# Kernel optimization log

Measured on AMD Instinct MI355X. Metric: run time of the kernel, lower is better.

The kernel has to match this reference:

```python
import jax, jax.numpy as jnp
import numpy as np

N, C, HW, HEADS = 2048, 16, 8, 4
F = C * HW * HW  # 1024
E = 16384
EPS = 1e-5
NEG_SLOPE = 0.2


def _bn(x, g, b):
    # training-mode BatchNorm2d over (N, H, W)
    m = x.mean(axis=(0, 2, 3), keepdims=True)
    v = x.var(axis=(0, 2, 3), keepdims=True)
    return (x - m) * jax.lax.rsqrt(v + EPS) * g[None, :, None, None] + b[None, :, None, None]


def _conv1x1(x, w, b):
    # 1x1 conv == per-pixel linear: w is [out_c, in_c]
    return jnp.einsum('nchw,oc->nohw', x, w) + b[None, :, None, None]


def _gatv2(xf, edge_index, wl, bl, wr, br, att, bias_gat):
    # xf: [N, F] node features
    xl = (xf @ wl + bl).reshape(N, HEADS, F)  # source-side transform (lin_l)
    xr = (xf @ wr + br).reshape(N, HEADS, F)  # target-side transform (lin_r)
    src, dst = edge_index[0], edge_index[1]
    loops = jnp.arange(N)
    # PyG default: remove existing self loops (mask them) then add self loops
    src_f = jnp.concatenate([src, loops])
    dst_f = jnp.concatenate([dst, loops])
    valid = jnp.concatenate([src != dst, jnp.ones((N,), bool)])
    xj = xl[src_f]                                   # [E+N, HEADS, F] gather
    e = jax.nn.leaky_relu(xj + xr[dst_f], negative_slope=NEG_SLOPE)
    logits = jnp.einsum('ehf,hf->eh', e, att)        # [E+N, HEADS]
    logits = jnp.where(valid[:, None], logits, -jnp.inf)
    mx = jax.lax.stop_gradient(jax.ops.segment_max(logits, dst_f, num_segments=N))
    expv = jnp.where(valid[:, None], jnp.exp(logits - mx[dst_f]), 0.0)
    denom = jax.ops.segment_sum(expv, dst_f, num_segments=N)
    alpha = expv / denom[dst_f]                      # segment softmax over incoming edges
    out = jax.ops.segment_sum(alpha[:, :, None] * xj, dst_f, num_segments=N)  # [N, HEADS, F]
    return out.reshape(N, HEADS * F) + bias_gat


def setup_inputs() -> dict:
    key = jax.random.key(0)
    ks = jax.random.split(key, 8)
    s = 0.02
    return {
        'x': jax.random.normal(ks[0], (N, C, HW, HW), jnp.float32),
        'edge_index': jax.random.randint(ks[1], (2, E), 0, N),
        'w1': jax.random.normal(ks[2], (C, C), jnp.float32) * s,
        'b1': jnp.zeros((C,), jnp.float32),
        'g1': jnp.ones((C,), jnp.float32),
        'be1': jnp.zeros((C,), jnp.float32),
        'wl': jax.random.normal(ks[3], (F, HEADS * F), jnp.float32) * s,
        'bl': jnp.zeros((HEADS * F,), jnp.float32),
        'wr': jax.random.normal(ks[4], (F, HEADS * F), jnp.float32) * s,
        'br': jnp.zeros((HEADS * F,), jnp.float32),
        'att': jax.random.normal(ks[5], (HEADS, F), jnp.float32) * s,
        'bias_gat': jnp.zeros((HEADS * F,), jnp.float32),
        'w2': jax.random.normal(ks[6], (C, HEADS * C), jnp.float32) * s,
        'b2': jnp.zeros((C,), jnp.float32),
        'g2': jnp.ones((C,), jnp.float32),
        'be2': jnp.zeros((C,), jnp.float32),
    }


def reference(x, edge_index, w1, b1, g1, be1, wl, bl, wr, br, att, bias_gat, w2, b2, g2, be2):
    res = x
    y = _bn(_conv1x1(x, w1, b1), g1, be1)            # fc1: Conv2d 1x1 + BN
    yf = y.reshape(N, F)
    g = _gatv2(yf, edge_index, wl, bl, wr, br, att, bias_gat)
    g = g.reshape(N, HEADS * C, HW, HW)
    out = _bn(_conv1x1(g, w2, b2), g2, be2)          # fc2: Conv2d 1x1 + BN
    return out + res                                  # DropPath(0.0) == Identity
```

## Files before the change

### kernel.cpp

```cpp
#include <hip/hip_runtime.h>
#include <stdint.h>

#define N_NODES 2048
#define F_DIM   1024
#define HEADS   4
#define NF      4096
#define ROW     8192
#define E_EDGES 16384
#define MAXE    (E_EDGES + N_NODES)
#define BN_EPS  1e-5f
#define NSLOPE  0.2f

typedef unsigned short ushort_t;
typedef __attribute__((ext_vector_type(8))) short bf16x8;
typedef __attribute__((ext_vector_type(4))) float f32x4;
typedef __attribute__((ext_vector_type(8))) unsigned short us8;

__device__ __forceinline__ float b2f(unsigned short u) {
    union { unsigned int i; float f; } x; x.i = ((unsigned int)u) << 16; return x.f;
}
__device__ __forceinline__ unsigned short f2b(float f) {
    union { float f; unsigned int i; } x; x.f = f;
    unsigned int r = x.i + 0x7fffu + ((x.i >> 16) & 1u);
    return (unsigned short)(r >> 16);
}
__device__ __forceinline__ ushort_t ld_canon(const void* src, size_t i, int f32) {
    return f32 ? f2b(((const float*)src)[i]) : ((const ushort_t*)src)[i];
}
__device__ __forceinline__ float ld_f(const void* src, size_t i, int f32) {
    return f32 ? ((const float*)src)[i] : b2f(((const ushort_t*)src)[i]);
}

__global__ __launch_bounds__(1024) void k_csr(
    const int* __restrict__ ei_raw, const ushort_t* __restrict__ x_probe,
    int* __restrict__ offs, int* __restrict__ esrc, int* __restrict__ flags)
{
    __shared__ int cnt[2048];
    __shared__ int ts[1024];
    __shared__ int sflag;
    int t = threadIdx.x;
    if (t < 64) {
        int nz = (ei_raw[2 * t + 1] != 0) ? 1 : 0;
        unsigned long long m = __ballot(nz);
        if (t == 0) sflag = (m == 0ull) ? 1 : 0;
    } else if (t >= 64 && t < 96) {
        unsigned e = (x_probe[2 * (t - 64)] >> 7) & 0xFF;
        unsigned long long m = __ballot(e >= 0x90u);
        if (t == 64) flags[0] = (__popcll(m) >= 3) ? 1 : 0;
    }
    cnt[t] = 0; cnt[t + 1024] = 0;
    __syncthreads();
    int i64 = sflag;
    for (int idx = t; idx < MAXE; idx += 1024) {
        if (idx < E_EDGES) {
            int s = i64 ? ei_raw[2 * idx] : ei_raw[idx];
            int d = i64 ? ei_raw[2 * (E_EDGES + idx)] : ei_raw[E_EDGES + idx];
            if (s != d) atomicAdd(&cnt[d], 1);
        } else {
            atomicAdd(&cnt[idx - E_EDGES], 1);
        }
    }
    __syncthreads();
    int l0 = cnt[2 * t], l1 = cnt[2 * t + 1], tot = l0 + l1;
    ts[t] = tot;
    __syncthreads();
    for (int s = 1; s < 1024; s <<= 1) {
        int v = (t >= s) ? ts[t - s] : 0;
        __syncthreads();
        ts[t] += v;
        __syncthreads();
    }
    int run = ts[t] - tot;
    offs[2 * t] = run; offs[2 * t + 1] = run + l0;
    if (t == 1023) offs[2048] = ts[1023];
    __syncthreads();
    cnt[2 * t] = run; cnt[2 * t + 1] = run + l0;
    __syncthreads();
    for (int idx = t; idx < MAXE; idx += 1024) {
        if (idx < E_EDGES) {
            int s = i64 ? ei_raw[2 * idx] : ei_raw[idx];
            int d = i64 ? ei_raw[2 * (E_EDGES + idx)] : ei_raw[E_EDGES + idx];
            if (s != d) esrc[atomicAdd(&cnt[d], 1)] = s;
        } else {
            int n = idx - E_EDGES;
            esrc[atomicAdd(&cnt[n], 1)] = n;
        }
    }
}

__global__ __launch_bounds__(256) void k_fc1(
    const void* __restrict__ x, const void* __restrict__ w1, const void* __restrict__ b1,
    const int* __restrict__ flags,
    float* __restrict__ y0, float* __restrict__ ps, float* __restrict__ pq)
{
    __shared__ float xs[1024];
    __shared__ float sw[256];
    __shared__ float sb[16];
    int f32 = flags[0];
    int tid = threadIdx.x;
    sw[tid] = ld_f(w1, tid, f32);
    if (tid < 16) sb[tid] = ld_f(b1, tid, f32);
    int wave = tid >> 6, lane = tid & 63;
    float s[4] = {0,0,0,0}, q[4] = {0,0,0,0};
    for (int nn = 0; nn < 8; ++nn) {
        int n = blockIdx.x * 8 + nn;
        __syncthreads();
        #pragma unroll
        for (int i = 0; i < 4; ++i) {
            int idx = tid + i * 256;
            xs[idx] = ld_f(x, (size_t)n * 1024 + idx, f32);
        }
        __syncthreads();
        #pragma unroll
        for (int i = 0; i < 4; ++i) {
            int o = wave * 4 + i;
            float acc = sb[o];
            #pragma unroll
            for (int c = 0; c < 16; ++c) acc += xs[c * 64 + lane] * sw[o * 16 + c];
            y0[(size_t)n * 1024 + o * 64 + lane] = acc;
            s[i] += acc; q[i] += acc * acc;
        }
    }
    #pragma unroll
    for (int i = 0; i < 4; ++i)
        for (int mm = 1; mm < 64; mm <<= 1) {
            s[i] += __shfl_xor(s[i], mm);
            q[i] += __shfl_xor(q[i], mm);
        }
    if (lane == 0)
        #pragma unroll
        for (int i = 0; i < 4; ++i) {
            ps[blockIdx.x * 16 + wave * 4 + i] = s[i];
            pq[blockIdx.x * 16 + wave * 4 + i] = q[i];
        }
}

__global__ __launch_bounds__(256) void k_norm(
    const float* __restrict__ y0, const float* __restrict__ ps, const float* __restrict__ pq,
    const void* __restrict__ g1, const void* __restrict__ be1, const int* __restrict__ flags,
    ushort_t* __restrict__ xf)
{
    __shared__ float red[2][64];
    __shared__ float scs[16], shs[16];
    int f32 = flags[0];
    int t = threadIdx.x, lane = t & 63, wv = t >> 6;
    float s = 0.f, q = 0.f;
    #pragma unroll
    for (int i = 0; i < 16; ++i) { s += ps[i * 256 + t]; q += pq[i * 256 + t]; }
    s += __shfl_xor(s, 16); q += __shfl_xor(q, 16);
    s += __shfl_xor(s, 32); q += __shfl_xor(q, 32);
    if (lane < 16) { red[0][wv * 16 + lane] = s; red[1][wv * 16 + lane] = q; }
    __syncthreads();
    if (t < 16) {
        float S = red[0][t] + red[0][16 + t] + red[0][32 + t] + red[0][48 + t];
        float Q = red[1][t] + red[1][16 + t] + red[1][32 + t] + red[1][48 + t];
        const float inv = 1.0f / 131072.0f;
        float mean = S * inv;
        float var  = Q * inv - mean * mean;
        float sc = ld_f(g1, t, f32) * rsqrtf(var + BN_EPS);
        scs[t] = sc;
        shs[t] = ld_f(be1, t, f32) - mean * sc;
    }
    __syncthreads();
    int base = blockIdx.x * 4096;
    #pragma unroll
    for (int i = 0; i < 16; ++i) {
        int k = base + t + i * 256;
        int ch = (k >> 6) & 15;
        xf[k] = f2b(y0[k] * scs[ch] + shs[ch]);
    }
}

__global__ __launch_bounds__(256) void k_convT(
    const void* __restrict__ wl, const void* __restrict__ wr,
    const int* __restrict__ flags, ushort_t* __restrict__ wT)
{
    __shared__ ushort_t tl[64][65];
    int f32 = flags[0];
    const void* in = blockIdx.z ? wr : wl;
    ushort_t* outT = wT + (size_t)blockIdx.z * 4194304ull;
    int bx = blockIdx.x * 64, by = blockIdx.y * 64;
    #pragma unroll
    for (int i = 0; i < 16; ++i) {
        int idx = threadIdx.x + i * 256;
        int r = idx >> 6, c = idx & 63;
        tl[r][c] = ld_canon(in, (size_t)(by + r) * 4096 + bx + c, f32);
    }
    __syncthreads();
    #pragma unroll
    for (int i = 0; i < 16; ++i) {
        int idx = threadIdx.x + i * 256;
        int r = idx >> 6, c = idx & 63;
        outT[(size_t)(bx + r) * 1024 + by + c] = tl[c][r];
    }
}

__global__ __launch_bounds__(256) void k_gemm(
    const ushort_t* __restrict__ A, const ushort_t* __restrict__ BT,
    const void* __restrict__ blr, const void* __restrict__ brr,
    const int* __restrict__ flags, ushort_t* __restrict__ out)
{
    __shared__ __align__(16) ushort_t smem[16384];
    ushort_t* As0 = smem;
    ushort_t* As1 = smem + 4096;
    ushort_t* Bs0 = smem + 8192;
    ushort_t* Bs1 = smem + 12288;
    ushort_t* cs  = smem;
    int f32 = flags[0];
    int tid = threadIdx.x;
    int wv = tid >> 6, ln = tid & 63;
    int m0 = blockIdx.y * 128, n0 = blockIdx.x * 128;
    int wm = (wv >> 1) * 64, wn = (wv & 1) * 64;
    int lr = ln & 15, quad = ln >> 4;

    f32x4 acc[4][4];
    #pragma unroll
    for (int i = 0; i < 4; ++i)
        #pragma unroll
        for (int j = 0; j < 4; ++j) acc[i][j] = (f32x4){0.f, 0.f, 0.f, 0.f};

    for (int k0 = 0; k0 < 1024; k0 += 64) {
        #pragma unroll
        for (int i = 0; i < 2; ++i) {
            int cbase = i * 256 + wv * 64;
            int ci = cbase + ln;
            int m = ci >> 2, kc = ci & 3;
            const ushort_t* ga = A + (size_t)(m0 + m) * 1024 + k0 + kc * 8;
            __builtin_amdgcn_global_load_lds(
                (const __attribute__((address_space(1))) void*)ga,
                (__attribute__((address_space(3))) void*)(&As0[cbase * 8]), 16, 0, 0);
            __builtin_amdgcn_global_load_lds(
                (const __attribute__((address_space(1))) void*)(ga + 32),
                (__attribute__((address_space(3))) void*)(&As1[cbase * 8]), 16, 0, 0);
            const ushort_t* gb = BT + (size_t)(n0 + m) * 1024 + k0 + kc * 8;
            __builtin_amdgcn_global_load_lds(
                (const __attribute__((address_space(1))) void*)gb,
                (__attribute__((address_space(3))) void*)(&Bs0[cbase * 8]), 16, 0, 0);
            __builtin_amdgcn_global_load_lds(
                (const __attribute__((address_space(1))) void*)(gb + 32),
                (__attribute__((address_space(3))) void*)(&Bs1[cbase * 8]), 16, 0, 0);
        }
        __syncthreads();
        #pragma unroll
        for (int p = 0; p < 2; ++p) {
            const ushort_t* Ap = p ? As1 : As0;
            const ushort_t* Bp = p ? Bs1 : Bs0;
            bf16x8 af[4], bfr[4];
            #pragma unroll
            for (int i = 0; i < 4; ++i)
                af[i] = *(const bf16x8*)(&Ap[(wm + i * 16 + lr) * 32 + quad * 8]);
            #pragma unroll
            for (int j = 0; j < 4; ++j)
                bfr[j] = *(const bf16x8*)(&Bp[(wn + j * 16 + lr) * 32 + quad * 8]);
            #pragma unroll
            for (int i = 0; i < 4; ++i)
                #pragma unroll
                for (int j = 0; j < 4; ++j)
                    acc[i][j] = __builtin_amdgcn_mfma_f32_16x16x32_bf16(af[i], bfr[j], acc[i][j], 0, 0, 0);
        }
        __syncthreads();
    }
    float bj[4];
    #pragma unroll
    for (int j = 0; j < 4; ++j) {
        int colg = n0 + wn + j * 16 + lr;
        bj[j] = (colg < 4096) ? ld_f(blr, colg, f32) : ld_f(brr, colg - 4096, f32);
    }
    #pragma unroll
    for (int ph = 0; ph < 2; ++ph) {
        if ((wv >> 1) == ph) {
            #pragma unroll
            for (int i = 0; i < 4; ++i)
                #pragma unroll
                for (int j = 0; j < 4; ++j) {
                    int col = wn + j * 16 + lr;
                    #pragma unroll
                    for (int r = 0; r < 4; ++r)
                        cs[(i * 16 + quad * 4 + r) * 136 + col] = f2b(acc[i][j][r] + bj[j]);
                }
        }
        __syncthreads();
        #pragma unroll
        for (int rr = 0; rr < 4; ++rr) {
            int slot = rr * 256 + tid;
            int row = slot >> 4, seg = slot & 15;
            us8 v = *(const us8*)&cs[row * 136 + seg * 8];
            *(us8*)(out + (size_t)(m0 + ph * 64 + row) * ROW + n0 + seg * 8) = v;
        }
        __syncthreads();
    }
}

__global__ __launch_bounds__(64) void k_gat(
    const ushort_t* __restrict__ xlr,
    const void* __restrict__ att, const void* __restrict__ bg,
    const int* __restrict__ flags,
    const int* __restrict__ offsets, const int* __restrict__ esrc,
    ushort_t* __restrict__ g)
{
    int bx = blockIdx.x;
    int d = bx >> 2, h = bx & 3;
    int l = threadIdx.x;
    int f32 = flags[0];
    int off = offsets[d], deg = offsets[d + 1] - off;
    size_t hF = (size_t)h * F_DIM + l * 16;

    float xrv[16], attv[16];
    {
        const ushort_t* xp = xlr + ((size_t)d * ROW + NF + hF);
        us8 x0 = *(const us8*)xp, x1 = *(const us8*)(xp + 8);
        #pragma unroll
        for (int j = 0; j < 8; ++j) {
            xrv[j] = b2f(x0[j]); xrv[8 + j] = b2f(x1[j]);
            attv[j]     = ld_f(att, hF + j, f32);
            attv[8 + j] = ld_f(att, hF + 8 + j, f32);
        }
    }
    float acc[16];
    #pragma unroll
    for (int j = 0; j < 16; ++j) acc[j] = 0.f;
    float s_run = 0.f;

    for (int c0 = 0; c0 < deg; c0 += 64) {
        int cnt = min(64, deg - c0);
        int eidx = esrc[off + c0 + (l < cnt ? l : 0)];
        int e = 0;
        for (; e + 3 < cnt; e += 4) {
            int i0 = __shfl(eidx, e),     i1 = __shfl(eidx, e + 1);
            int i2 = __shfl(eidx, e + 2), i3 = __shfl(eidx, e + 3);
            const ushort_t* p0 = xlr + ((size_t)i0 * ROW + hF);
            const ushort_t* p1 = xlr + ((size_t)i1 * ROW + hF);
            const ushort_t* p2 = xlr + ((size_t)i2 * ROW + hF);
            const ushort_t* p3 = xlr + ((size_t)i3 * ROW + hF);
            us8 v0[4], v1[4];
            v0[0] = *(const us8*)p0; v1[0] = *(const us8*)(p0 + 8);
            v0[1] = *(const us8*)p1; v1[1] = *(const us8*)(p1 + 8);
            v0[2] = *(const us8*)p2; v1[2] = *(const us8*)(p2 + 8);
            v0[3] = *(const us8*)p3; v1[3] = *(const us8*)(p3 + 8);
            float tt[4];
            #pragma unroll
            for (int k = 0; k < 4; ++k) {
                float t0 = 0.f;
                #pragma unroll
                for (int j = 0; j < 8; ++j) {
                    float u;
                    u = b2f(v0[k][j]) + xrv[j];     u = u > 0.f ? u : NSLOPE * u; t0 += u * attv[j];
                    u = b2f(v1[k][j]) + xrv[8 + j]; u = u > 0.f ? u : NSLOPE * u; t0 += u * attv[8 + j];
                }
                tt[k] = t0;
            }
            #pragma unroll
            for (int mm = 1; mm < 64; mm <<= 1) {
                tt[0] += __shfl_xor(tt[0], mm);
                tt[1] += __shfl_xor(tt[1], mm);
                tt[2] += __shfl_xor(tt[2], mm);
                tt[3] += __shfl_xor(tt[3], mm);
            }
            float w0 = __expf(tt[0]), w1 = __expf(tt[1]);
            float w2v = __expf(tt[2]), w3 = __expf(tt[3]);
            s_run += w0 + w1 + w2v + w3;
            #pragma unroll
            for (int j = 0; j < 8; ++j) {
                acc[j]     += w0 * b2f(v0[0][j]) + w1 * b2f(v0[1][j])
                            + w2v * b2f(v0[2][j]) + w3 * b2f(v0[3][j]);
                acc[8 + j] += w0 * b2f(v1[0][j]) + w1 * b2f(v1[1][j])
                            + w2v * b2f(v1[2][j]) + w3 * b2f(v1[3][j]);
            }
        }
        for (; e < cnt; ++e) {
            int i0 = __shfl(eidx, e);
            const ushort_t* p = xlr + ((size_t)i0 * ROW + hF);
            us8 a0 = *(const us8*)p, a1 = *(const us8*)(p + 8);
            float t0 = 0.f;
            #pragma unroll
            for (int j = 0; j < 8; ++j) {
                float u;
                u = b2f(a0[j]) + xrv[j];     u = u > 0.f ? u : NSLOPE * u; t0 += u * attv[j];
                u = b2f(a1[j]) + xrv[8 + j]; u = u > 0.f ? u : NSLOPE * u; t0 += u * attv[8 + j];
            }
            #pragma unroll
            for (int mm = 1; mm < 64; mm <<= 1) t0 += __shfl_xor(t0, mm);
            float w0 = __expf(t0);
            s_run += w0;
            #pragma unroll
            for (int j = 0; j < 8; ++j) {
                acc[j]     += w0 * b2f(a0[j]);
                acc[8 + j] += w0 * b2f(a1[j]);
            }
        }
    }
    float inv = 1.0f / s_run;
    ushort_t* gp = g + ((size_t)d * NF + hF);
    us8 outv0, outv1;
    #pragma unroll
    for (int j = 0; j < 8; ++j) {
        outv0[j] = f2b(acc[j] * inv + ld_f(bg, hF + j, f32));
        outv1[j] = f2b(acc[8 + j] * inv + ld_f(bg, hF + 8 + j, f32));
    }
    *(us8*)gp = outv0;
    *(us8*)(gp + 8) = outv1;
}

__global__ __launch_bounds__(256) void k_fc2(
    const ushort_t* __restrict__ g, const void* __restrict__ w2, const void* __restrict__ b2,
    const int* __restrict__ flags,
    float* __restrict__ z, float* __restrict__ ps, float* __restrict__ pq)
{
    __shared__ float gs[4096];
    __shared__ float sw[1024];
    __shared__ float sb[16];
    int f32 = flags[0];
    int tid = threadIdx.x;
    #pragma unroll
    for (int i = 0; i < 4; ++i) sw[tid + i * 256] = ld_f(w2, tid + i * 256, f32);
    if (tid < 16) sb[tid] = ld_f(b2, tid, f32);
    int wave = tid >> 6, lane = tid & 63;
    float s[4] = {0,0,0,0}, q[4] = {0,0,0,0};
    for (int nn = 0; nn < 8; ++nn) {
        int n = blockIdx.x * 8 + nn;
        __syncthreads();
        {
            const ushort_t* gp = g + (size_t)n * 4096 + tid * 16;
            us8 v0 = *(const us8*)gp, v1 = *(const us8*)(gp + 8);
            #pragma unroll
            for (int j = 0; j < 8; ++j) {
                gs[tid * 16 + j] = b2f(v0[j]);
                gs[tid * 16 + 8 + j] = b2f(v1[j]);
            }
        }
        __syncthreads();
        #pragma unroll
        for (int i = 0; i < 4; ++i) {
            int o = wave * 4 + i;
            float acc = sb[o];
            #pragma unroll
            for (int k = 0; k < 64; ++k) acc += gs[k * 64 + lane] * sw[o * 64 + k];
            z[(size_t)n * 1024 + o * 64 + lane] = acc;
            s[i] += acc; q[i] += acc * acc;
        }
    }
    #pragma unroll
    for (int i = 0; i < 4; ++i)
        for (int mm = 1; mm < 64; mm <<= 1) {
            s[i] += __shfl_xor(s[i], mm);
            q[i] += __shfl_xor(q[i], mm);
        }
    if (lane == 0)
        #pragma unroll
        for (int i = 0; i < 4; ++i) {
            ps[blockIdx.x * 16 + wave * 4 + i] = s[i];
            pq[blockIdx.x * 16 + wave * 4 + i] = q[i];
        }
}

__global__ __launch_bounds__(256) void k_out(
    const float* __restrict__ z, const void* __restrict__ x,
    const float* __restrict__ ps, const float* __restrict__ pq,
    const void* __restrict__ g2, const void* __restrict__ be2,
    const int* __restrict__ flags, void* __restrict__ out)
{
    __shared__ float red[2][64];
    __shared__ float scs[16], shs[16];
    int f32 = flags[0];
    int t = threadIdx.x, lane = t & 63, wv = t >> 6;
    float s = 0.f, q = 0.f;
    #pragma unroll
    for (int i = 0; i < 16; ++i) { s += ps[i * 256 + t]; q += pq[i * 256 + t]; }
    s += __shfl_xor(s, 16); q += __shfl_xor(q, 16);
    s += __shfl_xor(s, 32); q += __shfl_xor(q, 32);
    if (lane < 16) { red[0][wv * 16 + lane] = s; red[1][wv * 16 + lane] = q; }
    __syncthreads();
    if (t < 16) {
        float S = red[0][t] + red[0][16 + t] + red[0][32 + t] + red[0][48 + t];
        float Q = red[1][t] + red[1][16 + t] + red[1][32 + t] + red[1][48 + t];
        const float inv = 1.0f / 131072.0f;
        float mean = S * inv;
        float var  = Q * inv - mean * mean;
        float sc = ld_f(g2, t, f32) * rsqrtf(var + BN_EPS);
        scs[t] = sc;
        shs[t] = ld_f(be2, t, f32) - mean * sc;
    }
    __syncthreads();
    size_t base = (size_t)blockIdx.x * 8192;
    #pragma unroll
    for (int i = 0; i < 32; ++i) {
        size_t k = base + t + i * 256;
        int ch = ((int)k >> 6) & 15;
        float val = z[k] * scs[ch] + shs[ch] + ld_f(x, k, f32);
        if (f32) ((float*)out)[k] = val;
        else     ((ushort_t*)out)[k] = f2b(val);
    }
}

extern "C" void kernel_launch(void* const* d_in, const int* in_sizes, int n_in,
                              void* d_out, int out_size, void* d_ws, size_t ws_size,
                              hipStream_t stream)
{
    const void* x   = d_in[0];
    const void* ei  = d_in[1];
    const void* w1  = d_in[2];
    const void* b1  = d_in[3];
    const void* g1  = d_in[4];
    const void* be1 = d_in[5];
    const void* wl  = d_in[6];
    const void* bl  = d_in[7];
    const void* wr  = d_in[8];
    const void* br  = d_in[9];
    const void* att = d_in[10];
    const void* bg  = d_in[11];
    const void* w2  = d_in[12];
    const void* b2  = d_in[13];
    const void* g2  = d_in[14];
    const void* be2 = d_in[15];
    (void)in_sizes; (void)n_in; (void)out_size; (void)ws_size;

    char* wsb = (char*)d_ws;
    size_t o = 0;
    auto alloc = [&](size_t bytes) -> void* {
        void* p = wsb + o;
        o = (o + bytes + 255) & ~(size_t)255;
        return p;
    };
    int*      flags = (int*)alloc(256);
    float*    y0    = (float*)alloc(2097152ull * 4);
    float*    z     = y0;
    ushort_t* xf    = (ushort_t*)alloc(2097152ull * 2);
    ushort_t* wT    = (ushort_t*)alloc(8388608ull * 2);
    ushort_t* gbuf  = wT;
    ushort_t* xlr   = (ushort_t*)alloc(16777216ull * 2);
    float* p1s = (float*)alloc(256 * 16 * 4);
    float* p1q = (float*)alloc(256 * 16 * 4);
    float* p2s = (float*)alloc(256 * 16 * 4);
    float* p2q = (float*)alloc(256 * 16 * 4);
    int* offs  = (int*)alloc(2049 * 4);
    int* esrc  = (int*)alloc(MAXE * 4);

    k_csr<<<1, 1024, 0, stream>>>((const int*)ei, (const ushort_t*)x, offs, esrc, flags);
    k_fc1<<<256, 256, 0, stream>>>(x, w1, b1, flags, y0, p1s, p1q);
    k_norm<<<512, 256, 0, stream>>>(y0, p1s, p1q, g1, be1, flags, xf);
    k_convT<<<dim3(64, 16, 2), 256, 0, stream>>>(wl, wr, flags, wT);
    k_gemm<<<dim3(64, 16), 256, 0, stream>>>(xf, wT, bl, br, flags, xlr);
    k_gat<<<N_NODES * HEADS, 64, 0, stream>>>(xlr, att, bg, flags, offs, esrc, gbuf);
    k_fc2<<<256, 256, 0, stream>>>(gbuf, w2, b2, flags, z, p2s, p2q);
    k_out<<<256, 256, 0, stream>>>(z, x, p2s, p2q, g2, be2, flags, d_out);
}
```

Measured before the change: 286.6 us.

## Split single-block CSR build into parallel count/scan/scatter kernels; pack GAT heads per block

The single 1024-thread block that built the CSR is replaced by a memset plus three kernels: a multi-block atomic count into global memory, a one-block scan, and a multi-block scatter through a global cursor. The aim is to remove the serial one-CU bottleneck at the start of the pipeline. Separately, the GAT kernel now runs four (node, head) wavefronts per 256-thread block instead of one 64-thread block each, which cuts the block count. The cost is extra launches, global atomics instead of LDS atomics, and a nondeterministic edge order within each segment.

Result: no change. 290.7 us (+1.4%).

```diff
diff --git a/kernel.cpp b/kernel.cpp
--- a/kernel.cpp
+++ b/kernel.cpp
@@ -31,60 +31,75 @@
     return f32 ? ((const float*)src)[i] : b2f(((const ushort_t*)src)[i]);
 }
 
-__global__ __launch_bounds__(1024) void k_csr(
-    const int* __restrict__ ei_raw, const ushort_t* __restrict__ x_probe,
-    int* __restrict__ offs, int* __restrict__ esrc, int* __restrict__ flags)
-{
-    __shared__ int cnt[2048];
-    __shared__ int ts[1024];
-    __shared__ int sflag;
+__device__ __forceinline__ int sniff_i64(const int* ei_raw, int* lds_flag) {
     int t = threadIdx.x;
     if (t < 64) {
         int nz = (ei_raw[2 * t + 1] != 0) ? 1 : 0;
         unsigned long long m = __ballot(nz);
-        if (t == 0) sflag = (m == 0ull) ? 1 : 0;
-    } else if (t >= 64 && t < 96) {
+        if (t == 0) *lds_flag = (m == 0ull) ? 1 : 0;
+    }
+    __syncthreads();
+    return *lds_flag;
+}
+
+__global__ __launch_bounds__(256) void k_count(
+    const int* __restrict__ ei_raw, const ushort_t* __restrict__ x_probe,
+    int* __restrict__ counts, int* __restrict__ flags)
+{
+    __shared__ int sflag;
+    int i64 = sniff_i64(ei_raw, &sflag);
+    int t = threadIdx.x;
+    if (blockIdx.x == 0 && t >= 64 && t < 96) {
         unsigned e = (x_probe[2 * (t - 64)] >> 7) & 0xFF;
         unsigned long long m = __ballot(e >= 0x90u);
         if (t == 64) flags[0] = (__popcll(m) >= 3) ? 1 : 0;
     }
-    cnt[t] = 0; cnt[t + 1024] = 0;
-    __syncthreads();
-    int i64 = sflag;
-    for (int idx = t; idx < MAXE; idx += 1024) {
-        if (idx < E_EDGES) {
-            int s = i64 ? ei_raw[2 * idx] : ei_raw[idx];
-            int d = i64 ? ei_raw[2 * (E_EDGES + idx)] : ei_raw[E_EDGES + idx];
-            if (s != d) atomicAdd(&cnt[d], 1);
-        } else {
-            atomicAdd(&cnt[idx - E_EDGES], 1);
-        }
-    }
-    __syncthreads();
-    int l0 = cnt[2 * t], l1 = cnt[2 * t + 1], tot = l0 + l1;
-    ts[t] = tot;
-    __syncthreads();
-    for (int s = 1; s < 1024; s <<= 1) {
+    int idx = blockIdx.x * 256 + t;
+    if (idx < E_EDGES) {
+        int s = i64 ? ei_raw[2 * idx] : ei_raw[idx];
+        int d = i64 ? ei_raw[2 * (E_EDGES + idx)] : ei_raw[E_EDGES + idx];
+        if (s != d) atomicAdd(&counts[d], 1);
+    } else if (idx < MAXE) {
+        atomicAdd(&counts[idx - E_EDGES], 1);
+    }
+}
+
+__global__ __launch_bounds__(256) void k_scan(
+    const int* __restrict__ counts, int* __restrict__ offs, int* __restrict__ cursor)
+{
+    __shared__ int ts[256];
+    int t = threadIdx.x;
+    int loc[8]; int tot = 0;
+    #pragma unroll
+    for (int j = 0; j < 8; ++j) { loc[j] = counts[t * 8 + j]; tot += loc[j]; }
+    ts[t] = tot; __syncthreads();
+    for (int s = 1; s < 256; s <<= 1) {
         int v = (t >= s) ? ts[t - s] : 0;
         __syncthreads();
         ts[t] += v;
         __syncthreads();
     }
     int run = ts[t] - tot;
-    offs[2 * t] = run; offs[2 * t + 1] = run + l0;
-    if (t == 1023) offs[2048] = ts[1023];
-    __syncthreads();
-    cnt[2 * t] = run; cnt[2 * t + 1] = run + l0;
-    __syncthreads();
-    for (int idx = t; idx < MAXE; idx += 1024) {
-        if (idx < E_EDGES) {
-            int s = i64 ? ei_raw[2 * idx] : ei_raw[idx];
-            int d = i64 ? ei_raw[2 * (E_EDGES + idx)] : ei_raw[E_EDGES + idx];
-            if (s != d) esrc[atomicAdd(&cnt[d], 1)] = s;
-        } else {
-            int n = idx - E_EDGES;
-            esrc[atomicAdd(&cnt[n], 1)] = n;
-        }
+    #pragma unroll
+    for (int j = 0; j < 8; ++j) {
+        offs[t * 8 + j] = run; cursor[t * 8 + j] = run; run += loc[j];
+    }
+    if (t == 255) offs[2048] = run;
+}
+
+__global__ __launch_bounds__(256) void k_scatter(
+    const int* __restrict__ ei_raw, int* __restrict__ cursor, int* __restrict__ esrc)
+{
+    __shared__ int sflag;
+    int i64 = sniff_i64(ei_raw, &sflag);
+    int idx = blockIdx.x * 256 + threadIdx.x;
+    if (idx < E_EDGES) {
+        int s = i64 ? ei_raw[2 * idx] : ei_raw[idx];
+        int d = i64 ? ei_raw[2 * (E_EDGES + idx)] : ei_raw[E_EDGES + idx];
+        if (s != d) esrc[atomicAdd(&cursor[d], 1)] = s;
+    } else if (idx < MAXE) {
+        int n = idx - E_EDGES;
+        esrc[atomicAdd(&cursor[n], 1)] = n;
     }
 }
 
@@ -291,16 +306,16 @@
     }
 }
 
-__global__ __launch_bounds__(64) void k_gat(
+__global__ __launch_bounds__(256) void k_gat(
     const ushort_t* __restrict__ xlr,
     const void* __restrict__ att, const void* __restrict__ bg,
     const int* __restrict__ flags,
     const int* __restrict__ offsets, const int* __restrict__ esrc,
     ushort_t* __restrict__ g)
 {
-    int bx = blockIdx.x;
-    int d = bx >> 2, h = bx & 3;
-    int l = threadIdx.x;
+    int pair = blockIdx.x * 4 + (threadIdx.x >> 6);
+    int d = pair >> 2, h = pair & 3;
+    int l = threadIdx.x & 63;
     int f32 = flags[0];
     int off = offsets[d], deg = offsets[d + 1] - off;
     size_t hF = (size_t)h * F_DIM + l * 16;
@@ -532,15 +547,20 @@
     float* p1q = (float*)alloc(256 * 16 * 4);
     float* p2s = (float*)alloc(256 * 16 * 4);
     float* p2q = (float*)alloc(256 * 16 * 4);
-    int* offs  = (int*)alloc(2049 * 4);
-    int* esrc  = (int*)alloc(MAXE * 4);
-
-    k_csr<<<1, 1024, 0, stream>>>((const int*)ei, (const ushort_t*)x, offs, esrc, flags);
+    int* counts = (int*)alloc(2048 * 4);
+    int* offs   = (int*)alloc(2049 * 4);
+    int* cursor = (int*)alloc(2048 * 4);
+    int* esrc   = (int*)alloc(MAXE * 4);
+
+    hipMemsetAsync(counts, 0, 2048 * 4, stream);
+    k_count<<<72, 256, 0, stream>>>((const int*)ei, (const ushort_t*)x, counts, flags);
+    k_scan<<<1, 256, 0, stream>>>(counts, offs, cursor);
+    k_scatter<<<72, 256, 0, stream>>>((const int*)ei, cursor, esrc);
     k_fc1<<<256, 256, 0, stream>>>(x, w1, b1, flags, y0, p1s, p1q);
     k_norm<<<512, 256, 0, stream>>>(y0, p1s, p1q, g1, be1, flags, xf);
     k_convT<<<dim3(64, 16, 2), 256, 0, stream>>>(wl, wr, flags, wT);
     k_gemm<<<dim3(64, 16), 256, 0, stream>>>(xf, wT, bl, br, flags, xlr);
-    k_gat<<<N_NODES * HEADS, 64, 0, stream>>>(xlr, att, bg, flags, offs, esrc, gbuf);
+    k_gat<<<N_NODES, 256, 0, stream>>>(xlr, att, bg, flags, offs, esrc, gbuf);
     k_fc2<<<256, 256, 0, stream>>>(gbuf, w2, b2, flags, z, p2s, p2q);
     k_out<<<256, 256, 0, stream>>>(z, x, p2s, p2q, g2, be2, flags, d_out);
 }
```
